# Optimization experiments

Measured on AMD Instinct MI355X. Metric: run time of the kernel, lower is better.

The kernel has to match this reference:

```python
import jax, jax.numpy as jnp
import numpy as np
from jax import lax

B, L, D = 1, 2048, 768
D_IN, N, DT_RANK, K = 1536, 16, 48, 4
EPS = 1e-5


def setup_inputs() -> dict:
    key = jax.random.key(0)
    ks = jax.random.split(key, 10)
    s = 0.02
    x = jax.random.normal(ks[0], (B, L, D), dtype=jnp.float32)
    norm_w = jnp.ones((D,), dtype=jnp.float32)
    W_in = jax.random.normal(ks[1], (D, 2 * D_IN), dtype=jnp.float32) * s
    conv_w = jax.random.normal(ks[2], (K, 1, D_IN), dtype=jnp.float32) * s  # (W, I/groups, O)
    conv_b = jnp.zeros((D_IN,), dtype=jnp.float32)
    W_x = jax.random.normal(ks[3], (D_IN, DT_RANK + 2 * N), dtype=jnp.float32) * s
    W_dt = jax.random.normal(ks[4], (DT_RANK, D_IN), dtype=jnp.float32) * s
    b_dt = jnp.zeros((D_IN,), dtype=jnp.float32)
    A_log = jnp.broadcast_to(jnp.log(jnp.arange(1, N + 1, dtype=jnp.float32)), (D_IN, N))
    Dp = jnp.ones((D_IN,), dtype=jnp.float32)
    W_out = jax.random.normal(ks[5], (D_IN, D), dtype=jnp.float32) * s
    return {"x": x, "norm_w": norm_w, "W_in": W_in, "conv_w": conv_w, "conv_b": conv_b,
            "W_x": W_x, "W_dt": W_dt, "b_dt": b_dt, "A_log": A_log, "Dp": Dp, "W_out": W_out}


def _rmsnorm(x, w):
    return x * jax.lax.rsqrt(jnp.mean(x * x, axis=-1, keepdims=True) + EPS) * w


def _selective_scan(deltaA, deltaB_u, C):
    # deltaA, deltaB_u: (b, l, d_in, n); C: (b, l, n)
    def combine(s1, s2):
        f1, x1 = s1
        f2, x2 = s2
        return (f2 * f1, f2 * x1 + x2)
    _, xs = lax.associative_scan(combine, (deltaA, deltaB_u), axis=1)
    return jnp.einsum('bldn,bln->bld', xs, C)


def _mamba_block(x, W_in, conv_w, conv_b, W_x, W_dt, b_dt, A_log, Dp, W_out):
    b, l, d = x.shape
    xr = x @ W_in                                 # (b, l, 2*d_in)
    xs, res = jnp.split(xr, [D_IN], axis=-1)
    # depthwise causal-ish conv, padding = K-1 both sides, then trim to l
    xs = lax.conv_general_dilated(
        xs, conv_w, window_strides=(1,), padding=[(K - 1, K - 1)],
        dimension_numbers=('NWC', 'WIO', 'NWC'), feature_group_count=D_IN)
    xs = (xs + conv_b)[:, :l, :]
    u = jax.nn.silu(xs)
    # SSM
    A = -jnp.exp(A_log)                           # (d_in, n)
    x_dbl = u @ W_x                               # (b, l, dt_rank + 2n)
    delta, Bm, Cm = jnp.split(x_dbl, [DT_RANK, DT_RANK + N], axis=-1)
    delta = jax.nn.softplus(delta @ W_dt + b_dt)  # (b, l, d_in)
    deltaA = jnp.exp(jnp.einsum('bld,dn->bldn', delta, A))
    deltaB_u = jnp.einsum('bld,bln,bld->bldn', delta, Bm, u)
    y = _selective_scan(deltaA, deltaB_u, Cm) + u * Dp
    y = y * jax.nn.silu(res)
    return y @ W_out


def reference(x, norm_w, W_in, conv_w, conv_b, W_x, W_dt, b_dt, A_log, Dp, W_out):
    return _mamba_block(_rmsnorm(x, norm_w), W_in, conv_w, conv_b,
                        W_x, W_dt, b_dt, A_log, Dp, W_out) + x
```

## Files before the change

### kernel.cpp

```cpp
#include <hip/hip_runtime.h>
#include <hip/hip_bf16.h>

typedef unsigned short u16;
typedef __bf16 bfx8 __attribute__((ext_vector_type(8)));
typedef float fx4 __attribute__((ext_vector_type(4)));
typedef unsigned short ushort8 __attribute__((ext_vector_type(8)));

#define DEV __device__ __forceinline__

static constexpr int Lq = 2048, Dq = 768, DIN = 1536, NST = 16;
static constexpr int NCH = 64, LC = 32;

DEV u16 f2bf(float x) {
    union { float f; unsigned u; } v; v.f = x;
    unsigned r = v.u + 0x7fff + ((v.u >> 16) & 1);
    return (u16)(r >> 16);
}
DEV float bf2f(u16 v) {
    union { unsigned u; float f; } w; w.u = ((unsigned)v) << 16; return w.f;
}
DEV void gll16(const u16* g, u16* l) {
    __builtin_amdgcn_global_load_lds(
        (const __attribute__((address_space(1))) unsigned int*)g,
        (__attribute__((address_space(3))) unsigned int*)l, 16, 0, 0);
}

struct TD { const float* src; u16* dst; int R, C, Rp, Cp, nbx, blk0; };

__global__ __launch_bounds__(256) void transpose_all(TD t0, TD t1, TD t2, TD t3) {
    __shared__ float tile[32][33];
    TD td = t0;
    int b = blockIdx.x;
    if (b >= t3.blk0) td = t3; else if (b >= t2.blk0) td = t2; else if (b >= t1.blk0) td = t1;
    int local = b - td.blk0;
    int c0 = (local % td.nbx) * 32, r0 = (local / td.nbx) * 32;
    int tx = threadIdx.x & 31, ty = threadIdx.x >> 5;
    #pragma unroll
    for (int i = ty; i < 32; i += 8) {
        int r = r0 + i, c = c0 + tx;
        tile[i][tx] = (r < td.R && c < td.C) ? td.src[(size_t)r * td.C + c] : 0.f;
    }
    __syncthreads();
    #pragma unroll
    for (int i = ty; i < 32; i += 8) {
        int c = c0 + i, r = r0 + tx;
        if (c < td.Cp && r < td.Rp) td.dst[(size_t)c * td.Rp + r] = f2bf(tile[tx][i]);
    }
}

__global__ __launch_bounds__(256) void rmsnorm_kernel(const float* __restrict__ x,
                                                      const float* __restrict__ w,
                                                      u16* __restrict__ xn) {
    int t = blockIdx.x;
    const float* row = x + (size_t)t * Dq;
    float ss = 0.f;
    for (int i = threadIdx.x; i < Dq; i += 256) { float a = row[i]; ss += a * a; }
    #pragma unroll
    for (int o = 32; o > 0; o >>= 1) ss += __shfl_xor(ss, o, 64);
    __shared__ float wsum[4];
    if ((threadIdx.x & 63) == 0) wsum[threadIdx.x >> 6] = ss;
    __syncthreads();
    ss = wsum[0] + wsum[1] + wsum[2] + wsum[3];
    float scale = rsqrtf(ss * (1.f / Dq) + 1e-5f);
    for (int i = threadIdx.x; i < Dq; i += 256)
        xn[(size_t)t * Dq + i] = f2bf(row[i] * scale * w[i]);
}

template<int BM, int BN, int EPI>
__global__ __launch_bounds__(256) void gemm_nt(const u16* __restrict__ A, const u16* __restrict__ BT,
                                               float* __restrict__ C, u16* __restrict__ Cb,
                                               const float* __restrict__ R,
                                               const float* __restrict__ bias,
                                               int M, int N, int K) {
    constexpr int BK = 32;
    constexpr int WM = BM / 2, WN = BN / 2, MI = WM / 16, NI = WN / 16;
    __shared__ u16 As[BM * BK];
    __shared__ u16 Bs[BN * BK];
    const int tid = threadIdx.x, lane = tid & 63, wid = tid >> 6;
    const int wr = wid >> 1, wc = wid & 1;
    const int bm0 = blockIdx.y * BM, bn0 = blockIdx.x * BN;
    const int li = lane & 15, g = lane >> 4;

    fx4 acc[MI][NI];
    #pragma unroll
    for (int mi = 0; mi < MI; mi++)
        #pragma unroll
        for (int ni = 0; ni < NI; ni++)
            #pragma unroll
            for (int q = 0; q < 4; q++) acc[mi][ni][q] = 0.f;

    for (int kt = 0; kt < K; kt += BK) {
        #pragma unroll
        for (int i = 0; i < BM / 64; i++) {
            int c = (i * 4 + wid) * 64 + lane;
            gll16(A + (size_t)(bm0 + (c >> 2)) * K + kt + (c & 3) * 8, &As[(i * 4 + wid) * 512]);
        }
        #pragma unroll
        for (int i = 0; i < BN / 64; i++) {
            int c = (i * 4 + wid) * 64 + lane;
            gll16(BT + (size_t)(bn0 + (c >> 2)) * K + kt + (c & 3) * 8, &Bs[(i * 4 + wid) * 512]);
        }
        __syncthreads();
        bfx8 af[MI], bfr[NI];
        #pragma unroll
        for (int mi = 0; mi < MI; mi++) af[mi] = *(const bfx8*)&As[(wr * WM + mi * 16 + li) * BK + g * 8];
        #pragma unroll
        for (int ni = 0; ni < NI; ni++) bfr[ni] = *(const bfx8*)&Bs[(wc * WN + ni * 16 + li) * BK + g * 8];
        #pragma unroll
        for (int mi = 0; mi < MI; mi++)
            #pragma unroll
            for (int ni = 0; ni < NI; ni++)
                acc[mi][ni] = __builtin_amdgcn_mfma_f32_16x16x32_bf16(af[mi], bfr[ni], acc[mi][ni], 0, 0, 0);
        __syncthreads();
    }

    #pragma unroll
    for (int mi = 0; mi < MI; mi++)
        #pragma unroll
        for (int ni = 0; ni < NI; ni++)
            #pragma unroll
            for (int q = 0; q < 4; q++) {
                int row = bm0 + wr * WM + mi * 16 + g * 4 + q;
                int col = bn0 + wc * WN + ni * 16 + li;
                size_t idx = (size_t)row * N + col;
                float v = acc[mi][ni][q];
                if constexpr (EPI == 0) {
                    if (R) v += R[idx];
                    C[idx] = v;
                } else if constexpr (EPI == 3) {
                    Cb[idx] = f2bf(v);
                } else if constexpr (EPI == 4) {
                    v += bias[col];
                    Cb[idx] = f2bf((v > 20.f) ? v : log1pf(__expf(v)));
                } else if constexpr (EPI == 5) {
                    C[idx] = v;
                    if (col < 64) Cb[(size_t)row * 64 + col] = f2bf(v);
                }
            }
}

__global__ __launch_bounds__(256) void conv_silu(const u16* __restrict__ xrb,
                                                 const float* __restrict__ cw,
                                                 const float* __restrict__ cb,
                                                 u16* __restrict__ ubf) {
    int i = blockIdx.x * 256 + threadIdx.x;
    int t = i / (DIN / 8), d8 = (i - t * (DIN / 8)) * 8;
    float acc[8];
    #pragma unroll
    for (int j = 0; j < 8; j++) acc[j] = cb[d8 + j];
    #pragma unroll
    for (int k = 0; k < 4; k++) {
        int tt = t - 3 + k;
        if (tt < 0) continue;
        ushort8 xv = *(const ushort8*)(xrb + (size_t)tt * (2 * DIN) + d8);
        #pragma unroll
        for (int j = 0; j < 8; j++) acc[j] = fmaf(bf2f(xv[j]), cw[k * DIN + d8 + j], acc[j]);
    }
    ushort8 o;
    #pragma unroll
    for (int j = 0; j < 8; j++) {
        float s = acc[j] / (1.f + __expf(-acc[j]));
        o[j] = f2bf(s);
    }
    *(ushort8*)(ubf + (size_t)i * 8) = o;
}

__global__ __launch_bounds__(256) void scan_p1(const u16* __restrict__ deltab, const u16* __restrict__ ubf,
                                               const float* __restrict__ xdbl, const float* __restrict__ A_log,
                                               float* __restrict__ chA, float* __restrict__ chX) {
    int c = blockIdx.x;
    int d = blockIdx.y * 256 + threadIdx.x;
    float An[NST];
    #pragma unroll
    for (int i = 0; i < 4; i++) {
        float4 a = *(const float4*)(A_log + (size_t)d * NST + i * 4);
        An[i * 4 + 0] = -__expf(a.x); An[i * 4 + 1] = -__expf(a.y);
        An[i * 4 + 2] = -__expf(a.z); An[i * 4 + 3] = -__expf(a.w);
    }
    float s[NST];
    #pragma unroll
    for (int n = 0; n < NST; n++) s[n] = 0.f;
    float sdl = 0.f;
    int t0 = c * LC;
    for (int t = t0; t < t0 + LC; t++) {
        float dl = bf2f(deltab[(size_t)t * DIN + d]);
        float uu = bf2f(ubf[(size_t)t * DIN + d]);
        float dlu = dl * uu;
        float Bv[NST];
        #pragma unroll
        for (int i = 0; i < 4; i++) {
            float4 b = *(const float4*)(xdbl + (size_t)t * 128 + 48 + i * 4);
            Bv[i * 4 + 0] = b.x; Bv[i * 4 + 1] = b.y; Bv[i * 4 + 2] = b.z; Bv[i * 4 + 3] = b.w;
        }
        #pragma unroll
        for (int n = 0; n < NST; n++) {
            float dA = __expf(dl * An[n]);
            s[n] = fmaf(dA, s[n], dlu * Bv[n]);
        }
        sdl += dl;
    }
    size_t base = ((size_t)c * DIN + d) * NST;
    #pragma unroll
    for (int i = 0; i < 4; i++) {
        float4 v; v.x = s[i*4]; v.y = s[i*4+1]; v.z = s[i*4+2]; v.w = s[i*4+3];
        *(float4*)(chX + base + i * 4) = v;
    }
    #pragma unroll
    for (int i = 0; i < 4; i++) {
        float4 v;
        v.x = __expf(An[i*4+0] * sdl); v.y = __expf(An[i*4+1] * sdl);
        v.z = __expf(An[i*4+2] * sdl); v.w = __expf(An[i*4+3] * sdl);
        *(float4*)(chA + base + i * 4) = v;
    }
}

__global__ __launch_bounds__(256) void scan_p2(float* __restrict__ chA, const float* __restrict__ chX) {
    int i = blockIdx.x * 256 + threadIdx.x;
    float s = 0.f;
    for (int c = 0; c < NCH; c++) {
        size_t idx = (size_t)c * (DIN * NST) + i;
        float a = chA[idx], xv = chX[idx];
        chA[idx] = s;
        s = fmaf(a, s, xv);
    }
}

__global__ __launch_bounds__(256) void scan_p3(const u16* __restrict__ deltab, const u16* __restrict__ ubf,
                                               const float* __restrict__ xdbl, const float* __restrict__ A_log,
                                               const float* __restrict__ init, const float* __restrict__ Dp,
                                               const u16* __restrict__ xrb, u16* __restrict__ ybf) {
    int c = blockIdx.x;
    int d = blockIdx.y * 256 + threadIdx.x;
    float An[NST];
    #pragma unroll
    for (int i = 0; i < 4; i++) {
        float4 a = *(const float4*)(A_log + (size_t)d * NST + i * 4);
        An[i * 4 + 0] = -__expf(a.x); An[i * 4 + 1] = -__expf(a.y);
        An[i * 4 + 2] = -__expf(a.z); An[i * 4 + 3] = -__expf(a.w);
    }
    float s[NST];
    size_t base = ((size_t)c * DIN + d) * NST;
    #pragma unroll
    for (int i = 0; i < 4; i++) {
        float4 v = *(const float4*)(init + base + i * 4);
        s[i * 4 + 0] = v.x; s[i * 4 + 1] = v.y; s[i * 4 + 2] = v.z; s[i * 4 + 3] = v.w;
    }
    float Dpd = Dp[d];
    int t0 = c * LC;
    for (int t = t0; t < t0 + LC; t++) {
        float dl = bf2f(deltab[(size_t)t * DIN + d]);
        float uu = bf2f(ubf[(size_t)t * DIN + d]);
        float dlu = dl * uu;
        float Bv[NST], Cv[NST];
        #pragma unroll
        for (int i = 0; i < 4; i++) {
            float4 b = *(const float4*)(xdbl + (size_t)t * 128 + 48 + i * 4);
            Bv[i * 4 + 0] = b.x; Bv[i * 4 + 1] = b.y; Bv[i * 4 + 2] = b.z; Bv[i * 4 + 3] = b.w;
            float4 cc = *(const float4*)(xdbl + (size_t)t * 128 + 64 + i * 4);
            Cv[i * 4 + 0] = cc.x; Cv[i * 4 + 1] = cc.y; Cv[i * 4 + 2] = cc.z; Cv[i * 4 + 3] = cc.w;
        }
        float p = 0.f;
        #pragma unroll
        for (int n = 0; n < NST; n++) {
            float dA = __expf(dl * An[n]);
            s[n] = fmaf(dA, s[n], dlu * Bv[n]);
            p = fmaf(s[n], Cv[n], p);
        }
        float res = bf2f(xrb[(size_t)t * (2 * DIN) + DIN + d]);
        float y = fmaf(uu, Dpd, p) * (res / (1.f + __expf(-res)));
        ybf[(size_t)t * DIN + d] = f2bf(y);
    }
}

extern "C" void kernel_launch(void* const* d_in, const int* in_sizes, int n_in,
                              void* d_out, int out_size, void* d_ws, size_t ws_size,
                              hipStream_t stream) {
    const float* x      = (const float*)d_in[0];
    const float* norm_w = (const float*)d_in[1];
    const float* W_in   = (const float*)d_in[2];
    const float* conv_w = (const float*)d_in[3];
    const float* conv_b = (const float*)d_in[4];
    const float* W_x    = (const float*)d_in[5];
    const float* W_dt   = (const float*)d_in[6];
    const float* b_dt   = (const float*)d_in[7];
    const float* A_log  = (const float*)d_in[8];
    const float* Dp     = (const float*)d_in[9];
    const float* W_out  = (const float*)d_in[10];
    float* out = (float*)d_out;

    char* wp = (char*)d_ws;
    auto alloc = [&](size_t bytes) { char* p = wp; wp += (bytes + 255) & ~(size_t)255; return p; };
    u16*   WinT   = (u16*)alloc((size_t)3072 * 768 * 2);
    u16*   WoutT  = (u16*)alloc((size_t)768 * 1536 * 2);
    u16*   WxT    = (u16*)alloc((size_t)128 * 1536 * 2);
    u16*   WdtT   = (u16*)alloc((size_t)1536 * 64 * 2);
    u16*   xn     = (u16*)alloc((size_t)Lq * Dq * 2);
    u16*   xrb    = (u16*)alloc((size_t)Lq * 3072 * 2);
    u16*   ubf    = (u16*)alloc((size_t)Lq * DIN * 2);
    float* xdbl   = (float*)alloc((size_t)Lq * 128 * 4);
    u16*   draw   = (u16*)alloc((size_t)Lq * 64 * 2);
    u16*   deltab = (u16*)alloc((size_t)Lq * DIN * 2);
    float* chA    = (float*)alloc((size_t)NCH * DIN * NST * 4);
    float* chX    = (float*)alloc((size_t)NCH * DIN * NST * 4);
    u16*   ybf    = (u16*)alloc((size_t)Lq * DIN * 2);
    (void)ws_size; (void)in_sizes; (void)n_in; (void)out_size;

    TD t0{W_in,  WinT,  768, 3072,  768, 3072, 96,    0};
    TD t1{W_out, WoutT, 1536, 768, 1536,  768, 24, 2304};
    TD t2{W_x,   WxT,  1536,   80, 1536,  128,  4, 3456};
    TD t3{W_dt,  WdtT,   48, 1536,   64, 1536, 48, 3648};
    transpose_all<<<3744, 256, 0, stream>>>(t0, t1, t2, t3);

    rmsnorm_kernel<<<Lq, 256, 0, stream>>>(x, norm_w, xn);

    gemm_nt<128, 128, 3><<<dim3(3072 / 128, Lq / 128), 256, 0, stream>>>(
        xn, WinT, nullptr, xrb, nullptr, nullptr, Lq, 3072, 768);

    conv_silu<<<(Lq * DIN / 8) / 256, 256, 0, stream>>>(xrb, conv_w, conv_b, ubf);

    gemm_nt<64, 64, 5><<<dim3(128 / 64, Lq / 64), 256, 0, stream>>>(
        ubf, WxT, xdbl, draw, nullptr, nullptr, Lq, 128, DIN);

    gemm_nt<128, 128, 4><<<dim3(1536 / 128, Lq / 128), 256, 0, stream>>>(
        draw, WdtT, nullptr, deltab, nullptr, b_dt, Lq, DIN, 64);

    scan_p1<<<dim3(NCH, DIN / 256), 256, 0, stream>>>(deltab, ubf, xdbl, A_log, chA, chX);
    scan_p2<<<(DIN * NST) / 256, 256, 0, stream>>>(chA, chX);
    scan_p3<<<dim3(NCH, DIN / 256), 256, 0, stream>>>(deltab, ubf, xdbl, A_log, chA, Dp, xrb, ybf);

    gemm_nt<64, 64, 0><<<dim3(Dq / 64, Lq / 64), 256, 0, stream>>>(
        ybf, WoutT, out, nullptr, x, nullptr, Lq, Dq, DIN);
}
```

Baseline: 244.9 us.

## Fuse prep kernels, merge scan phases with grid barrier, swizzle GEMM LDS with BK=64

Merges the weight transposes and RMSNorm into one launch, and fuses the three selective-scan phases into a single kernel. The fused scan uses a software grid barrier built on atomics, with chunk count doubled to 128 and per-thread delta/u cached in registers. The GEMM K-tile grows to 64 with XOR-swizzled LDS layout to reduce bank conflicts, and the output GEMM uses a 128x64 tile. The grid barrier assumes all 768 scan blocks are co-resident, which risks deadlock or contention, and adds spin-wait overhead.

After: 891.7 us. 3.64x slower.

```diff
diff --git a/kernel.cpp b/kernel.cpp
--- a/kernel.cpp
+++ b/kernel.cpp
@@ -9,7 +9,8 @@
 #define DEV __device__ __forceinline__
 
 static constexpr int Lq = 2048, Dq = 768, DIN = 1536, NST = 16;
-static constexpr int NCH = 64, LC = 32;
+static constexpr int NCH = 128, LC = 16;
+static constexpr int SCB = NCH * (DIN / 256);
 
 DEV u16 f2bf(float x) {
     union { float f; unsigned u; } v; v.f = x;
@@ -25,45 +26,64 @@
         (__attribute__((address_space(3))) unsigned int*)l, 16, 0, 0);
 }
 
+DEV void softbar(unsigned* cnt, unsigned* flag, unsigned nblk) {
+    __syncthreads();
+    if (threadIdx.x == 0) {
+        __threadfence();
+        unsigned a = __hip_atomic_fetch_add(cnt, 1u, __ATOMIC_ACQ_REL, __HIP_MEMORY_SCOPE_AGENT);
+        if (a == nblk - 1u) {
+            __hip_atomic_store(flag, 1u, __ATOMIC_RELEASE, __HIP_MEMORY_SCOPE_AGENT);
+        } else {
+            while (__hip_atomic_load(flag, __ATOMIC_ACQUIRE, __HIP_MEMORY_SCOPE_AGENT) == 0u)
+                __builtin_amdgcn_s_sleep(8);
+        }
+        __threadfence();
+    }
+    __syncthreads();
+}
+
 struct TD { const float* src; u16* dst; int R, C, Rp, Cp, nbx, blk0; };
 
-__global__ __launch_bounds__(256) void transpose_all(TD t0, TD t1, TD t2, TD t3) {
+__global__ __launch_bounds__(256) void prep(TD t0, TD t1, TD t2, TD t3,
+                                            const float* __restrict__ x,
+                                            const float* __restrict__ nw,
+                                            u16* __restrict__ xn,
+                                            unsigned* __restrict__ bar) {
     __shared__ float tile[32][33];
-    TD td = t0;
+    __shared__ float wsum[4];
     int b = blockIdx.x;
-    if (b >= t3.blk0) td = t3; else if (b >= t2.blk0) td = t2; else if (b >= t1.blk0) td = t1;
-    int local = b - td.blk0;
-    int c0 = (local % td.nbx) * 32, r0 = (local / td.nbx) * 32;
-    int tx = threadIdx.x & 31, ty = threadIdx.x >> 5;
-    #pragma unroll
-    for (int i = ty; i < 32; i += 8) {
-        int r = r0 + i, c = c0 + tx;
-        tile[i][tx] = (r < td.R && c < td.C) ? td.src[(size_t)r * td.C + c] : 0.f;
-    }
-    __syncthreads();
-    #pragma unroll
-    for (int i = ty; i < 32; i += 8) {
-        int c = c0 + i, r = r0 + tx;
-        if (c < td.Cp && r < td.Rp) td.dst[(size_t)c * td.Rp + r] = f2bf(tile[tx][i]);
-    }
-}
-
-__global__ __launch_bounds__(256) void rmsnorm_kernel(const float* __restrict__ x,
-                                                      const float* __restrict__ w,
-                                                      u16* __restrict__ xn) {
-    int t = blockIdx.x;
-    const float* row = x + (size_t)t * Dq;
-    float ss = 0.f;
-    for (int i = threadIdx.x; i < Dq; i += 256) { float a = row[i]; ss += a * a; }
-    #pragma unroll
-    for (int o = 32; o > 0; o >>= 1) ss += __shfl_xor(ss, o, 64);
-    __shared__ float wsum[4];
-    if ((threadIdx.x & 63) == 0) wsum[threadIdx.x >> 6] = ss;
-    __syncthreads();
-    ss = wsum[0] + wsum[1] + wsum[2] + wsum[3];
-    float scale = rsqrtf(ss * (1.f / Dq) + 1e-5f);
-    for (int i = threadIdx.x; i < Dq; i += 256)
-        xn[(size_t)t * Dq + i] = f2bf(row[i] * scale * w[i]);
+    if (b == 0 && threadIdx.x < 8) bar[threadIdx.x] = 0;
+    if (b < 3744) {
+        TD td = t0;
+        if (b >= t3.blk0) td = t3; else if (b >= t2.blk0) td = t2; else if (b >= t1.blk0) td = t1;
+        int local = b - td.blk0;
+        int c0 = (local % td.nbx) * 32, r0 = (local / td.nbx) * 32;
+        int tx = threadIdx.x & 31, ty = threadIdx.x >> 5;
+        #pragma unroll
+        for (int i = ty; i < 32; i += 8) {
+            int r = r0 + i, c = c0 + tx;
+            tile[i][tx] = (r < td.R && c < td.C) ? td.src[(size_t)r * td.C + c] : 0.f;
+        }
+        __syncthreads();
+        #pragma unroll
+        for (int i = ty; i < 32; i += 8) {
+            int c = c0 + i, r = r0 + tx;
+            if (c < td.Cp && r < td.Rp) td.dst[(size_t)c * td.Rp + r] = f2bf(tile[tx][i]);
+        }
+    } else {
+        int t = b - 3744;
+        const float* row = x + (size_t)t * Dq;
+        float ss = 0.f;
+        for (int i = threadIdx.x; i < Dq; i += 256) { float a = row[i]; ss += a * a; }
+        #pragma unroll
+        for (int o = 32; o > 0; o >>= 1) ss += __shfl_xor(ss, o, 64);
+        if ((threadIdx.x & 63) == 0) wsum[threadIdx.x >> 6] = ss;
+        __syncthreads();
+        ss = wsum[0] + wsum[1] + wsum[2] + wsum[3];
+        float scale = rsqrtf(ss * (1.f / Dq) + 1e-5f);
+        for (int i = threadIdx.x; i < Dq; i += 256)
+            xn[(size_t)t * Dq + i] = f2bf(row[i] * scale * nw[i]);
+    }
 }
 
 template<int BM, int BN, int EPI>
@@ -72,7 +92,7 @@
                                                const float* __restrict__ R,
                                                const float* __restrict__ bias,
                                                int M, int N, int K) {
-    constexpr int BK = 32;
+    constexpr int BK = 64;
     constexpr int WM = BM / 2, WN = BN / 2, MI = WM / 16, NI = WN / 16;
     __shared__ u16 As[BM * BK];
     __shared__ u16 Bs[BN * BK];
@@ -91,26 +111,43 @@
 
     for (int kt = 0; kt < K; kt += BK) {
         #pragma unroll
-        for (int i = 0; i < BM / 64; i++) {
-            int c = (i * 4 + wid) * 64 + lane;
-            gll16(A + (size_t)(bm0 + (c >> 2)) * K + kt + (c & 3) * 8, &As[(i * 4 + wid) * 512]);
-        }
-        #pragma unroll
-        for (int i = 0; i < BN / 64; i++) {
-            int c = (i * 4 + wid) * 64 + lane;
-            gll16(BT + (size_t)(bn0 + (c >> 2)) * K + kt + (c & 3) * 8, &Bs[(i * 4 + wid) * 512]);
+        for (int i = 0; i < (BM * 8) / 256; i++) {
+            int cb = i * 256 + wid * 64;
+            int c = cb + lane;
+            int row = c >> 3, c16 = (c & 7) ^ (row & 7);
+            gll16(A + (size_t)(bm0 + row) * K + kt + c16 * 8, &As[cb * 8]);
+        }
+        #pragma unroll
+        for (int i = 0; i < (BN * 8) / 256; i++) {
+            int cb = i * 256 + wid * 64;
+            int c = cb + lane;
+            int row = c >> 3, c16 = (c & 7) ^ (row & 7);
+            gll16(BT + (size_t)(bn0 + row) * K + kt + c16 * 8, &Bs[cb * 8]);
         }
         __syncthreads();
-        bfx8 af[MI], bfr[NI];
-        #pragma unroll
-        for (int mi = 0; mi < MI; mi++) af[mi] = *(const bfx8*)&As[(wr * WM + mi * 16 + li) * BK + g * 8];
-        #pragma unroll
-        for (int ni = 0; ni < NI; ni++) bfr[ni] = *(const bfx8*)&Bs[(wc * WN + ni * 16 + li) * BK + g * 8];
-        #pragma unroll
-        for (int mi = 0; mi < MI; mi++)
-            #pragma unroll
-            for (int ni = 0; ni < NI; ni++)
-                acc[mi][ni] = __builtin_amdgcn_mfma_f32_16x16x32_bf16(af[mi], bfr[ni], acc[mi][ni], 0, 0, 0);
+        bfx8 af[MI][2], bfr[NI][2];
+        #pragma unroll
+        for (int mi = 0; mi < MI; mi++) {
+            int row = wr * WM + mi * 16 + li;
+            #pragma unroll
+            for (int ks = 0; ks < 2; ks++)
+                af[mi][ks] = *(const bfx8*)&As[row * BK + (((ks * 4 + g) ^ (row & 7)) * 8)];
+        }
+        #pragma unroll
+        for (int ni = 0; ni < NI; ni++) {
+            int row = wc * WN + ni * 16 + li;
+            #pragma unroll
+            for (int ks = 0; ks < 2; ks++)
+                bfr[ni][ks] = *(const bfx8*)&Bs[row * BK + (((ks * 4 + g) ^ (row & 7)) * 8)];
+        }
+        #pragma unroll
+        for (int ks = 0; ks < 2; ks++)
+            #pragma unroll
+            for (int mi = 0; mi < MI; mi++)
+                #pragma unroll
+                for (int ni = 0; ni < NI; ni++)
+                    acc[mi][ni] = __builtin_amdgcn_mfma_f32_16x16x32_bf16(
+                        af[mi][ks], bfr[ni][ks], acc[mi][ni], 0, 0, 0);
         __syncthreads();
     }
 
@@ -165,11 +202,15 @@
     *(ushort8*)(ubf + (size_t)i * 8) = o;
 }
 
-__global__ __launch_bounds__(256) void scan_p1(const u16* __restrict__ deltab, const u16* __restrict__ ubf,
-                                               const float* __restrict__ xdbl, const float* __restrict__ A_log,
-                                               float* __restrict__ chA, float* __restrict__ chX) {
-    int c = blockIdx.x;
-    int d = blockIdx.y * 256 + threadIdx.x;
+__global__ __launch_bounds__(256, 4) void scan_fused(
+        const u16* __restrict__ deltab, const u16* __restrict__ ubf,
+        const float* __restrict__ xdbl, const float* __restrict__ A_log,
+        const float* __restrict__ Dp, const u16* __restrict__ xrb,
+        float* __restrict__ chA, float* __restrict__ chX,
+        unsigned* __restrict__ bar, u16* __restrict__ ybf) {
+    const int c = blockIdx.x;
+    const int d = blockIdx.y * 256 + threadIdx.x;
+    const int fid = blockIdx.y * NCH + blockIdx.x;
     float An[NST];
     #pragma unroll
     for (int i = 0; i < 4; i++) {
@@ -180,91 +221,66 @@
     float s[NST];
     #pragma unroll
     for (int n = 0; n < NST; n++) s[n] = 0.f;
-    float sdl = 0.f;
-    int t0 = c * LC;
-    for (int t = t0; t < t0 + LC; t++) {
+    float dlr[LC], uur[LC], sdl = 0.f;
+    const int t0 = c * LC;
+    #pragma unroll
+    for (int tt = 0; tt < LC; tt++) {
+        int t = t0 + tt;
         float dl = bf2f(deltab[(size_t)t * DIN + d]);
         float uu = bf2f(ubf[(size_t)t * DIN + d]);
+        dlr[tt] = dl; uur[tt] = uu;
         float dlu = dl * uu;
-        float Bv[NST];
         #pragma unroll
         for (int i = 0; i < 4; i++) {
             float4 b = *(const float4*)(xdbl + (size_t)t * 128 + 48 + i * 4);
-            Bv[i * 4 + 0] = b.x; Bv[i * 4 + 1] = b.y; Bv[i * 4 + 2] = b.z; Bv[i * 4 + 3] = b.w;
-        }
-        #pragma unroll
-        for (int n = 0; n < NST; n++) {
-            float dA = __expf(dl * An[n]);
-            s[n] = fmaf(dA, s[n], dlu * Bv[n]);
+            float dA0 = __expf(dl * An[i*4+0]); s[i*4+0] = fmaf(dA0, s[i*4+0], dlu * b.x);
+            float dA1 = __expf(dl * An[i*4+1]); s[i*4+1] = fmaf(dA1, s[i*4+1], dlu * b.y);
+            float dA2 = __expf(dl * An[i*4+2]); s[i*4+2] = fmaf(dA2, s[i*4+2], dlu * b.z);
+            float dA3 = __expf(dl * An[i*4+3]); s[i*4+3] = fmaf(dA3, s[i*4+3], dlu * b.w);
         }
         sdl += dl;
     }
-    size_t base = ((size_t)c * DIN + d) * NST;
-    #pragma unroll
-    for (int i = 0; i < 4; i++) {
-        float4 v; v.x = s[i*4]; v.y = s[i*4+1]; v.z = s[i*4+2]; v.w = s[i*4+3];
-        *(float4*)(chX + base + i * 4) = v;
-    }
-    #pragma unroll
-    for (int i = 0; i < 4; i++) {
-        float4 v;
-        v.x = __expf(An[i*4+0] * sdl); v.y = __expf(An[i*4+1] * sdl);
-        v.z = __expf(An[i*4+2] * sdl); v.w = __expf(An[i*4+3] * sdl);
-        *(float4*)(chA + base + i * 4) = v;
-    }
-}
-
-__global__ __launch_bounds__(256) void scan_p2(float* __restrict__ chA, const float* __restrict__ chX) {
-    int i = blockIdx.x * 256 + threadIdx.x;
-    float s = 0.f;
-    for (int c = 0; c < NCH; c++) {
-        size_t idx = (size_t)c * (DIN * NST) + i;
-        float a = chA[idx], xv = chX[idx];
-        chA[idx] = s;
-        s = fmaf(a, s, xv);
-    }
-}
-
-__global__ __launch_bounds__(256) void scan_p3(const u16* __restrict__ deltab, const u16* __restrict__ ubf,
-                                               const float* __restrict__ xdbl, const float* __restrict__ A_log,
-                                               const float* __restrict__ init, const float* __restrict__ Dp,
-                                               const u16* __restrict__ xrb, u16* __restrict__ ybf) {
-    int c = blockIdx.x;
-    int d = blockIdx.y * 256 + threadIdx.x;
-    float An[NST];
-    #pragma unroll
-    for (int i = 0; i < 4; i++) {
-        float4 a = *(const float4*)(A_log + (size_t)d * NST + i * 4);
-        An[i * 4 + 0] = -__expf(a.x); An[i * 4 + 1] = -__expf(a.y);
-        An[i * 4 + 2] = -__expf(a.z); An[i * 4 + 3] = -__expf(a.w);
-    }
-    float s[NST];
-    size_t base = ((size_t)c * DIN + d) * NST;
-    #pragma unroll
-    for (int i = 0; i < 4; i++) {
-        float4 v = *(const float4*)(init + base + i * 4);
-        s[i * 4 + 0] = v.x; s[i * 4 + 1] = v.y; s[i * 4 + 2] = v.z; s[i * 4 + 3] = v.w;
+    #pragma unroll
+    for (int n = 0; n < NST; n++) {
+        size_t idx = (size_t)n * (NCH * DIN) + (size_t)c * DIN + d;
+        __hip_atomic_store(&chX[idx], s[n], __ATOMIC_RELAXED, __HIP_MEMORY_SCOPE_AGENT);
+        __hip_atomic_store(&chA[idx], __expf(An[n] * sdl), __ATOMIC_RELAXED, __HIP_MEMORY_SCOPE_AGENT);
+    }
+    softbar(&bar[0], &bar[1], SCB);
+    if (fid < 96) {
+        int n = fid / 6, dblk = fid % 6;
+        int dd = dblk * 256 + threadIdx.x;
+        size_t base = (size_t)n * (NCH * DIN) + dd;
+        float s2 = 0.f;
+        for (int cc = 0; cc < NCH; cc++) {
+            size_t idx = base + (size_t)cc * DIN;
+            float a  = __hip_atomic_load(&chA[idx], __ATOMIC_RELAXED, __HIP_MEMORY_SCOPE_AGENT);
+            float xv = __hip_atomic_load(&chX[idx], __ATOMIC_RELAXED, __HIP_MEMORY_SCOPE_AGENT);
+            __hip_atomic_store(&chA[idx], s2, __ATOMIC_RELAXED, __HIP_MEMORY_SCOPE_AGENT);
+            s2 = fmaf(a, s2, xv);
+        }
+    }
+    softbar(&bar[2], &bar[3], SCB);
+    #pragma unroll
+    for (int n = 0; n < NST; n++) {
+        size_t idx = (size_t)n * (NCH * DIN) + (size_t)c * DIN + d;
+        s[n] = __hip_atomic_load(&chA[idx], __ATOMIC_RELAXED, __HIP_MEMORY_SCOPE_AGENT);
     }
     float Dpd = Dp[d];
-    int t0 = c * LC;
-    for (int t = t0; t < t0 + LC; t++) {
-        float dl = bf2f(deltab[(size_t)t * DIN + d]);
-        float uu = bf2f(ubf[(size_t)t * DIN + d]);
+    #pragma unroll
+    for (int tt = 0; tt < LC; tt++) {
+        int t = t0 + tt;
+        float dl = dlr[tt], uu = uur[tt];
         float dlu = dl * uu;
-        float Bv[NST], Cv[NST];
+        float p = 0.f;
         #pragma unroll
         for (int i = 0; i < 4; i++) {
-            float4 b = *(const float4*)(xdbl + (size_t)t * 128 + 48 + i * 4);
-            Bv[i * 4 + 0] = b.x; Bv[i * 4 + 1] = b.y; Bv[i * 4 + 2] = b.z; Bv[i * 4 + 3] = b.w;
+            float4 b  = *(const float4*)(xdbl + (size_t)t * 128 + 48 + i * 4);
             float4 cc = *(const float4*)(xdbl + (size_t)t * 128 + 64 + i * 4);
-            Cv[i * 4 + 0] = cc.x; Cv[i * 4 + 1] = cc.y; Cv[i * 4 + 2] = cc.z; Cv[i * 4 + 3] = cc.w;
-        }
-        float p = 0.f;
-        #pragma unroll
-        for (int n = 0; n < NST; n++) {
-            float dA = __expf(dl * An[n]);
-            s[n] = fmaf(dA, s[n], dlu * Bv[n]);
-            p = fmaf(s[n], Cv[n], p);
+            float dA0 = __expf(dl * An[i*4+0]); s[i*4+0] = fmaf(dA0, s[i*4+0], dlu * b.x); p = fmaf(s[i*4+0], cc.x, p);
+            float dA1 = __expf(dl * An[i*4+1]); s[i*4+1] = fmaf(dA1, s[i*4+1], dlu * b.y); p = fmaf(s[i*4+1], cc.y, p);
+            float dA2 = __expf(dl * An[i*4+2]); s[i*4+2] = fmaf(dA2, s[i*4+2], dlu * b.z); p = fmaf(s[i*4+2], cc.z, p);
+            float dA3 = __expf(dl * An[i*4+3]); s[i*4+3] = fmaf(dA3, s[i*4+3], dlu * b.w); p = fmaf(s[i*4+3], cc.w, p);
         }
         float res = bf2f(xrb[(size_t)t * (2 * DIN) + DIN + d]);
         float y = fmaf(uu, Dpd, p) * (res / (1.f + __expf(-res)));
@@ -290,28 +306,27 @@
 
     char* wp = (char*)d_ws;
     auto alloc = [&](size_t bytes) { char* p = wp; wp += (bytes + 255) & ~(size_t)255; return p; };
-    u16*   WinT   = (u16*)alloc((size_t)3072 * 768 * 2);
-    u16*   WoutT  = (u16*)alloc((size_t)768 * 1536 * 2);
-    u16*   WxT    = (u16*)alloc((size_t)128 * 1536 * 2);
-    u16*   WdtT   = (u16*)alloc((size_t)1536 * 64 * 2);
-    u16*   xn     = (u16*)alloc((size_t)Lq * Dq * 2);
-    u16*   xrb    = (u16*)alloc((size_t)Lq * 3072 * 2);
-    u16*   ubf    = (u16*)alloc((size_t)Lq * DIN * 2);
-    float* xdbl   = (float*)alloc((size_t)Lq * 128 * 4);
-    u16*   draw   = (u16*)alloc((size_t)Lq * 64 * 2);
-    u16*   deltab = (u16*)alloc((size_t)Lq * DIN * 2);
-    float* chA    = (float*)alloc((size_t)NCH * DIN * NST * 4);
-    float* chX    = (float*)alloc((size_t)NCH * DIN * NST * 4);
-    u16*   ybf    = (u16*)alloc((size_t)Lq * DIN * 2);
+    u16*      WinT   = (u16*)alloc((size_t)3072 * 768 * 2);
+    u16*      WoutT  = (u16*)alloc((size_t)768 * 1536 * 2);
+    u16*      WxT    = (u16*)alloc((size_t)128 * 1536 * 2);
+    u16*      WdtT   = (u16*)alloc((size_t)1536 * 64 * 2);
+    u16*      xn     = (u16*)alloc((size_t)Lq * Dq * 2);
+    u16*      xrb    = (u16*)alloc((size_t)Lq * 3072 * 2);
+    u16*      ubf    = (u16*)alloc((size_t)Lq * DIN * 2);
+    float*    xdbl   = (float*)alloc((size_t)Lq * 128 * 4);
+    u16*      draw   = (u16*)alloc((size_t)Lq * 64 * 2);
+    u16*      deltab = (u16*)alloc((size_t)Lq * DIN * 2);
+    float*    chA    = (float*)alloc((size_t)NCH * DIN * NST * 4);
+    float*    chX    = (float*)alloc((size_t)NCH * DIN * NST * 4);
+    u16*      ybf    = (u16*)alloc((size_t)Lq * DIN * 2);
+    unsigned* bar    = (unsigned*)alloc(256);
     (void)ws_size; (void)in_sizes; (void)n_in; (void)out_size;
 
     TD t0{W_in,  WinT,  768, 3072,  768, 3072, 96,    0};
     TD t1{W_out, WoutT, 1536, 768, 1536,  768, 24, 2304};
     TD t2{W_x,   WxT,  1536,   80, 1536,  128,  4, 3456};
     TD t3{W_dt,  WdtT,   48, 1536,   64, 1536, 48, 3648};
-    transpose_all<<<3744, 256, 0, stream>>>(t0, t1, t2, t3);
-
-    rmsnorm_kernel<<<Lq, 256, 0, stream>>>(x, norm_w, xn);
+    prep<<<3744 + Lq, 256, 0, stream>>>(t0, t1, t2, t3, x, norm_w, xn, bar);
 
     gemm_nt<128, 128, 3><<<dim3(3072 / 128, Lq / 128), 256, 0, stream>>>(
         xn, WinT, nullptr, xrb, nullptr, nullptr, Lq, 3072, 768);
@@ -324,10 +339,9 @@
     gemm_nt<128, 128, 4><<<dim3(1536 / 128, Lq / 128), 256, 0, stream>>>(
         draw, WdtT, nullptr, deltab, nullptr, b_dt, Lq, DIN, 64);
 
-    scan_p1<<<dim3(NCH, DIN / 256), 256, 0, stream>>>(deltab, ubf, xdbl, A_log, chA, chX);
-    scan_p2<<<(DIN * NST) / 256, 256, 0, stream>>>(chA, chX);
-    scan_p3<<<dim3(NCH, DIN / 256), 256, 0, stream>>>(deltab, ubf, xdbl, A_log, chA, Dp, xrb, ybf);
-
-    gemm_nt<64, 64, 0><<<dim3(Dq / 64, Lq / 64), 256, 0, stream>>>(
+    scan_fused<<<dim3(NCH, DIN / 256), 256, 0, stream>>>(
+        deltab, ubf, xdbl, A_log, Dp, xrb, chA, chX, bar, ybf);
+
+    gemm_nt<128, 64, 0><<<dim3(Dq / 64, Lq / 128), 256, 0, stream>>>(
         ybf, WoutT, out, nullptr, x, nullptr, Lq, Dq, DIN);
 }
```
